# Kernel optimization log

Measured on AMD Instinct MI355X. Metric: run time of the kernel, lower is better.

## Reference

```python
import jax, jax.numpy as jnp
import numpy as np

W_LEN = 10

def _mlp3(x, W1, b1, W2, b2, W3, b3):
    x = jax.nn.relu(x @ W1 + b1)
    x = jax.nn.relu(x @ W2 + b2)
    return x @ W3 + b3

def _make_params(key):
    ks = jax.random.split(key, 16)
    def lin(k, i, o):
        k1, k2 = jax.random.split(k)
        s = 1.0 / np.sqrt(i)
        return (jax.random.uniform(k1, (i, o), jnp.float32, -s, s),
                jax.random.uniform(k2, (o,), jnp.float32, -s, s))
    p = {}
    # encoder: (obs+act)*W = 400 -> 64 -> 64 -> 2
    p['enc_W1'], p['enc_b1'] = lin(ks[0], 400, 64)
    p['enc_W2'], p['enc_b2'] = lin(ks[1], 64, 64)
    p['enc_W3'], p['enc_b3'] = lin(ks[2], 64, 2)
    # GRUCell: input = action+stoch = 10, hidden = det = 2; gates r,z,n
    s = 1.0 / np.sqrt(2)
    p['gru_Wih'] = jax.random.uniform(ks[3], (10, 6), jnp.float32, -s, s)
    p['gru_Whh'] = jax.random.uniform(ks[4], (2, 6), jnp.float32, -s, s)
    p['gru_bih'] = jax.random.uniform(ks[5], (6,), jnp.float32, -s, s)
    p['gru_bhh'] = jax.random.uniform(ks[6], (6,), jnp.float32, -s, s)
    # post_mlp: 2 -> 16 -> 16 -> 2
    p['post_W1'], p['post_b1'] = lin(ks[7], 2, 16)
    p['post_W2'], p['post_b2'] = lin(ks[8], 16, 16)
    p['post_W3'], p['post_b3'] = lin(ks[9], 16, 2)
    # decoder: stoch+action = 10 -> 64 -> 64 -> obs_dim
    p['dec_W1'], p['dec_b1'] = lin(ks[10], 10, 64)
    p['dec_W2'], p['dec_b2'] = lin(ks[11], 64, 64)
    p['dec_W3'], p['dec_b3'] = lin(ks[12], 64, 32)
    return p

def setup_inputs() -> dict:
    key = jax.random.key(0)
    k1, k2, k3, k4, k5 = jax.random.split(key, 5)
    B, T, OD, AD = 512, 512, 32, 8
    N = T - W_LEN + 1
    inp = {
        'obs': jax.random.normal(k1, (B, T, OD), jnp.float32),
        'action': jax.random.normal(k2, (B, T, AD), jnp.float32),
        't_label': jax.random.randint(k3, (B, T), 0, 10, jnp.int32),
        'mask': jax.random.randint(k4, (B, N), 0, 2, jnp.int32),
    }
    inp.update(_make_params(k5))
    return inp

def reference(obs, action, t_label, mask,
              enc_W1, enc_b1, enc_W2, enc_b2, enc_W3, enc_b3,
              gru_Wih, gru_Whh, gru_bih, gru_bhh,
              post_W1, post_b1, post_W2, post_b2, post_W3, post_b3,
              dec_W1, dec_b1, dec_W2, dec_b2, dec_W3, dec_b3):
    B, T, OD = obs.shape
    AD = action.shape[-1]
    N = T - W_LEN + 1
    DET = gru_Whh.shape[0]

    oa = jnp.concatenate([obs, action], axis=-1)            # [B,T,C]
    target_obs_traj = obs[:, W_LEN - 1:, :]                  # [B,N,OD]
    action_traj = action[:, W_LEN - 1:, :]                   # [B,N,AD]
    labels = t_label[:, W_LEN - 1:]

    # torch unfold(1, W, 1): [B,N,C,W] with window along last axis, flatten c-major
    idx = jnp.arange(N)[:, None] + jnp.arange(W_LEN)[None, :]  # [N,W]
    win = oa[:, idx, :]                                      # [B,N,W,C]
    win = jnp.swapaxes(win, 2, 3).reshape(B, N, -1)          # [B,N,C*W]
    priors = _mlp3(win, enc_W1, enc_b1, enc_W2, enc_b2, enc_W3, enc_b3)  # [B,N,S]

    x0 = jnp.zeros((B, DET), obs.dtype)
    s0 = priors[:, 0, :]

    def step(carry, xs):
        x_prev, s_prev = carry
        prior_t, a_t, m_t = xs
        m = m_t[:, None].astype(x_prev.dtype)
        st = m * prior_t + (1.0 - m) * s_prev
        gin = jnp.concatenate([a_t, st], axis=-1)
        gi = gin @ gru_Wih + gru_bih
        gh = x_prev @ gru_Whh + gru_bhh
        ir, iz, inn = jnp.split(gi, 3, axis=-1)
        hr, hz, hn = jnp.split(gh, 3, axis=-1)
        r = jax.nn.sigmoid(ir + hr)
        z = jax.nn.sigmoid(iz + hz)
        n = jnp.tanh(inn + r * hn)
        x_new = (1.0 - z) * n + z * x_prev
        s_new = _mlp3(x_new, post_W1, post_b1, post_W2, post_b2, post_W3, post_b3)
        return (x_new, s_new), (x_new, s_new)

    xs = (jnp.swapaxes(priors[:, :N - 1, :], 0, 1),
          jnp.swapaxes(action_traj[:, :N - 1, :], 0, 1),
          jnp.swapaxes(mask[:, :N - 1], 0, 1))
    _, (x_seq, s_seq) = jax.lax.scan(step, (x0, s0), xs)
    x_traj = jnp.concatenate([x0[:, None, :], jnp.swapaxes(x_seq, 0, 1)], axis=1)  # [B,N,DET]
    posts = jnp.concatenate([s0[:, None, :], jnp.swapaxes(s_seq, 0, 1)], axis=1)   # [B,N,S]

    post_obs_pred = _mlp3(jnp.concatenate([posts, action_traj], axis=-1),
                          dec_W1, dec_b1, dec_W2, dec_b2, dec_W3, dec_b3)          # [B,N,OD]
    return (post_obs_pred, priors, posts, x_traj, target_obs_traj, labels)
```

## Files before the change

kernel.cpp:

```cpp
#include <hip/hip_runtime.h>
#include <hip/hip_bf16.h>

namespace {

constexpr int Bb = 512;
constexpr int Tt = 512;
constexpr int OD = 32;
constexpr int AD = 8;
constexpr int WL = 10;
constexpr int Nn = Tt - WL + 1;
constexpr int CH = OD + AD;
constexpr int REC_T = 512;

constexpr float LOG2E = 1.4426950408889634f;

constexpr long SZ_PO = (long)Bb * Nn * 32;
constexpr long SZ_PR = (long)Bb * Nn * 2;
constexpr long OFF_POST   = 0;
constexpr long OFF_PRIORS = SZ_PO;
constexpr long OFF_POSTS  = OFF_PRIORS + SZ_PR;
constexpr long OFF_XTRAJ  = OFF_POSTS + SZ_PR;
constexpr long OFF_TGT    = OFF_XTRAJ + SZ_PR;
constexpr long OFF_LAB    = OFF_TGT + SZ_PO;

constexpr int PK_W1  = 0;
constexpr int PK_W2  = 26624;
constexpr int PK_W3  = 30720;
constexpr int PK_DW1 = 31744;
constexpr int PK_DW2 = 33792;
constexpr int PK_DW3 = 37888;
constexpr int PK_TOTAL = 39936;

typedef __attribute__((ext_vector_type(8))) short bf16x8;
typedef __attribute__((ext_vector_type(4))) float f32x4;

__device__ __align__(16) short g_pack[PK_TOTAL];

__device__ __forceinline__ f32x4 mfma16(bf16x8 a, bf16x8 b, f32x4 c) {
  return __builtin_amdgcn_mfma_f32_16x16x32_bf16(a, b, c, 0, 0, 0);
}

__device__ __forceinline__ unsigned short f2bf(float x) {
  unsigned int u = __float_as_uint(x);
  unsigned int r = u + 0x7fffu + ((u >> 16) & 1u);
  return (unsigned short)(r >> 16);
}

__device__ __forceinline__ float sigmoidf_(float x) {
  return 1.0f / (1.0f + __expf(-x));
}
__device__ __forceinline__ float tanh_(float x) {
  return 1.0f - 2.0f / (__expf(2.0f * x) + 1.0f);
}

template <int CTRL>
__device__ __forceinline__ float dpp_add(float x) {
  int y = __builtin_amdgcn_update_dpp(0, __float_as_int(x), CTRL, 0xf, 0xf, false);
  return x + __int_as_float(y);
}
template <int CTRL>
__device__ __forceinline__ float dpp_mov(float x) {
  return __int_as_float(
      __builtin_amdgcn_update_dpp(0, __float_as_int(x), CTRL, 0xf, 0xf, false));
}
__device__ __forceinline__ float row16_allsum(float x) {
  x = dpp_add<0xB1>(x);
  x = dpp_add<0x4E>(x);
  x = dpp_add<0x141>(x);
  x = dpp_add<0x140>(x);
  return x;
}

__global__ __launch_bounds__(256) void pack_kernel(
    const float* __restrict__ W1, const float* __restrict__ W2,
    const float* __restrict__ W3, const float* __restrict__ dW1,
    const float* __restrict__ dW2, const float* __restrict__ dW3) {
  const int idx = blockIdx.x * 256 + threadIdx.x;
  if (idx >= PK_TOTAL) return;
  float v = 0.0f;
  int base, r;
  if (idx < PK_W2) {
    base = PK_W1; r = idx - base;
    const int frag = r >> 9, inner = r & 511;
    const int lane = inner >> 3, j = inner & 7;
    const int kb = frag >> 2, jb = frag & 3;
    const int col = lane & 15;
    const int kp = kb * 32 + ((lane >> 4) << 3) + j;
    if (kp < 400) {
      const int w = kp / 40, c = kp - w * 40;
      v = W1[(c * 10 + w) * 64 + jb * 16 + col];
    }
  } else if (idx < PK_W3) {
    base = PK_W2; r = idx - base;
    const int frag = r >> 9, inner = r & 511;
    const int lane = inner >> 3, j = inner & 7;
    const int kb = frag >> 2, jb = frag & 3;
    const int col = lane & 15;
    const int k = kb * 32 + ((lane >> 4) << 3) + j;
    v = W2[k * 64 + jb * 16 + col];
  } else if (idx < PK_DW1) {
    base = PK_W3; r = idx - base;
    const int frag = r >> 9, inner = r & 511;
    const int lane = inner >> 3, j = inner & 7;
    const int kb = frag;
    const int col = lane & 15;
    const int k = kb * 32 + ((lane >> 4) << 3) + j;
    v = (col < 2) ? W3[k * 2 + col] : 0.0f;
  } else if (idx < PK_DW2) {
    base = PK_DW1; r = idx - base;
    const int frag = r >> 9, inner = r & 511;
    const int lane = inner >> 3, j = inner & 7;
    const int jb = frag;
    const int col = lane & 15;
    const int k = ((lane >> 4) << 3) + j;
    v = (k < 10) ? dW1[k * 64 + jb * 16 + col] : 0.0f;
  } else if (idx < PK_DW3) {
    base = PK_DW2; r = idx - base;
    const int frag = r >> 9, inner = r & 511;
    const int lane = inner >> 3, j = inner & 7;
    const int kb = frag >> 2, jb = frag & 3;
    const int col = lane & 15;
    const int k = kb * 32 + ((lane >> 4) << 3) + j;
    v = dW2[k * 64 + jb * 16 + col];
  } else {
    base = PK_DW3; r = idx - base;
    const int frag = r >> 9, inner = r & 511;
    const int lane = inner >> 3, j = inner & 7;
    const int kb = frag >> 1, jb = frag & 1;
    const int col = lane & 15;
    const int k = kb * 32 + ((lane >> 4) << 3) + j;
    v = dW3[k * 32 + jb * 16 + col];
  }
  g_pack[idx] = (short)f2bf(v);
}

__global__ void copy_kernel(const float* __restrict__ obs,
                            const int* __restrict__ tlab,
                            float* __restrict__ out) {
  const int total4 = (int)(SZ_PO / 4);
  const int totalL = Bb * Nn;
  const int stride = gridDim.x * blockDim.x;
  float4* out4 = reinterpret_cast<float4*>(out + OFF_TGT);
  const float4* obs4 = reinterpret_cast<const float4*>(obs);
  for (int idx = blockIdx.x * blockDim.x + threadIdx.x;
       idx < total4 + totalL; idx += stride) {
    if (idx < total4) {
      const int b = idx / (Nn * 8);
      const int r = idx - b * (Nn * 8);
      const int n = r >> 3;
      const int c4 = r & 7;
      out4[idx] = obs4[((long)b * Tt + n + WL - 1) * 8 + c4];
    } else {
      const int j = idx - total4;
      const int b = j / Nn;
      const int n = j - b * Nn;
      out[OFF_LAB + j] = (float)tlab[(long)b * Tt + n + WL - 1];
    }
  }
}

__global__ __launch_bounds__(256) void enc_mfma(
    const float* __restrict__ obs, const float* __restrict__ act,
    const float* __restrict__ b1, const float* __restrict__ b2,
    const float* __restrict__ b3, float* __restrict__ out) {
  __shared__ __align__(16) unsigned short sA[74 * 40];
  __shared__ __align__(16) unsigned short sH1[64 * 64];
  __shared__ __align__(16) unsigned short sH2[64 * 64];
  const int b = blockIdx.x >> 3;
  const int n0 = (blockIdx.x & 7) << 6;
  const int tid = threadIdx.x;
  const int lane = tid & 63, wv = tid >> 6;
  const int q = lane >> 4, lr = lane & 15;
  const int nl = wv * 16 + lr;

  for (int e = tid; e < 74 * 40; e += 256) {
    const int row = e / 40, c = e - row * 40;
    int t = n0 + row; t = t < Tt ? t : Tt - 1;
    const float v = (c < OD) ? obs[((long)b * Tt + t) * OD + c]
                             : act[((long)b * Tt + t) * AD + c - OD];
    sA[e] = f2bf(v);
  }
  __syncthreads();

  const char* sAb = (const char*)sA;
  f32x4 acc[4] = {{0,0,0,0},{0,0,0,0},{0,0,0,0},{0,0,0,0}};
  {
    int c0 = q * 8, w = 0;
#pragma unroll
    for (int kb = 0; kb < 13; ++kb) {
      const bf16x8 a = *(const bf16x8*)(sAb + (nl + w) * 80 + c0 * 2);
#pragma unroll
      for (int jb = 0; jb < 4; ++jb) {
        const bf16x8 bw =
            *(const bf16x8*)&g_pack[PK_W1 + ((kb * 4 + jb) * 64 + lane) * 8];
        acc[jb] = mfma16(a, bw, acc[jb]);
      }
      c0 += 32;
      if (c0 >= 40) { c0 -= 40; ++w; }
    }
  }
  {
#pragma unroll
    for (int jb = 0; jb < 4; ++jb) {
      const float bb = b1[jb * 16 + lr];
#pragma unroll
      for (int r = 0; r < 4; ++r) {
        const int grow = wv * 16 + q * 4 + r;
        const int col = jb * 16 + lr;
        const float v = fmaxf(acc[jb][r] + bb, 0.0f);
        const int byte = (grow * 128 + col * 2) ^ ((grow & 7) << 4);
        *(unsigned short*)((char*)sH1 + byte) = f2bf(v);
      }
    }
  }
  __syncthreads();

  f32x4 ac2[4] = {{0,0,0,0},{0,0,0,0},{0,0,0,0},{0,0,0,0}};
#pragma unroll
  for (int kb = 0; kb < 2; ++kb) {
    const int byte = (nl * 128 + kb * 64 + q * 16) ^ ((lr & 7) << 4);
    const bf16x8 a = *(const bf16x8*)((const char*)sH1 + byte);
#pragma unroll
    for (int jb = 0; jb < 4; ++jb) {
      const bf16x8 bw =
          *(const bf16x8*)&g_pack[PK_W2 + ((kb * 4 + jb) * 64 + lane) * 8];
      ac2[jb] = mfma16(a, bw, ac2[jb]);
    }
  }
  {
#pragma unroll
    for (int jb = 0; jb < 4; ++jb) {
      const float bb = b2[jb * 16 + lr];
#pragma unroll
      for (int r = 0; r < 4; ++r) {
        const int grow = wv * 16 + q * 4 + r;
        const int col = jb * 16 + lr;
        const float v = fmaxf(ac2[jb][r] + bb, 0.0f);
        const int byte = (grow * 128 + col * 2) ^ ((grow & 7) << 4);
        *(unsigned short*)((char*)sH2 + byte) = f2bf(v);
      }
    }
  }
  __syncthreads();

  f32x4 ac3 = {0, 0, 0, 0};
#pragma unroll
  for (int kb = 0; kb < 2; ++kb) {
    const int byte = (nl * 128 + kb * 64 + q * 16) ^ ((lr & 7) << 4);
    const bf16x8 a = *(const bf16x8*)((const char*)sH2 + byte);
    const bf16x8 bw = *(const bf16x8*)&g_pack[PK_W3 + (kb * 64 + lane) * 8];
    ac3 = mfma16(a, bw, ac3);
  }
  if (lr < 2) {
    const float bb = b3[lr];
#pragma unroll
    for (int r = 0; r < 4; ++r) {
      const int grow = wv * 16 + q * 4 + r;
      const int n = n0 + grow;
      if (n < Nn) out[OFF_PRIORS + ((long)b * Nn + n) * 2 + lr] = ac3[r] + bb;
    }
  }
}

__global__ __launch_bounds__(256) void dec_mfma(
    const float* __restrict__ act, const float* __restrict__ b1,
    const float* __restrict__ b2, const float* __restrict__ b3,
    float* __restrict__ out) {
  __shared__ __align__(16) unsigned short sD[64 * 32];
  __shared__ __align__(16) unsigned short sH1[64 * 64];
  __shared__ __align__(16) unsigned short sH2[64 * 64];
  const int b = blockIdx.x >> 3;
  const int n0 = (blockIdx.x & 7) << 6;
  const int tid = threadIdx.x;
  const int lane = tid & 63, wv = tid >> 6;
  const int q = lane >> 4, lr = lane & 15;
  const int nl = wv * 16 + lr;
  const float* posts = out + OFF_POSTS;

  for (int e = tid; e < 64 * 32; e += 256) {
    const int row = e >> 5, c = e & 31;
    int n = n0 + row; n = n < Nn ? n : Nn - 1;
    float v = 0.0f;
    if (c < 2) v = posts[((long)b * Nn + n) * 2 + c];
    else if (c < 10) v = act[((long)b * Tt + n + WL - 1) * AD + c - 2];
    const int byte = (row * 64 + c * 2) ^ ((row & 3) << 4);
    *(unsigned short*)((char*)sD + byte) = f2bf(v);
  }
  __syncthreads();

  f32x4 acc[4] = {{0,0,0,0},{0,0,0,0},{0,0,0,0},{0,0,0,0}};
  {
    const int byte = (nl * 64 + q * 16) ^ ((nl & 3) << 4);
    const bf16x8 a = *(const bf16x8*)((const char*)sD + byte);
#pragma unroll
    for (int jb = 0; jb < 4; ++jb) {
      const bf16x8 bw = *(const bf16x8*)&g_pack[PK_DW1 + (jb * 64 + lane) * 8];
      acc[jb] = mfma16(a, bw, acc[jb]);
    }
  }
  {
#pragma unroll
    for (int jb = 0; jb < 4; ++jb) {
      const float bb = b1[jb * 16 + lr];
#pragma unroll
      for (int r = 0; r < 4; ++r) {
        const int grow = wv * 16 + q * 4 + r;
        const int col = jb * 16 + lr;
        const float v = fmaxf(acc[jb][r] + bb, 0.0f);
        const int byte = (grow * 128 + col * 2) ^ ((grow & 7) << 4);
        *(unsigned short*)((char*)sH1 + byte) = f2bf(v);
      }
    }
  }
  __syncthreads();

  f32x4 ac2[4] = {{0,0,0,0},{0,0,0,0},{0,0,0,0},{0,0,0,0}};
#pragma unroll
  for (int kb = 0; kb < 2; ++kb) {
    const int byte = (nl * 128 + kb * 64 + q * 16) ^ ((lr & 7) << 4);
    const bf16x8 a = *(const bf16x8*)((const char*)sH1 + byte);
#pragma unroll
    for (int jb = 0; jb < 4; ++jb) {
      const bf16x8 bw =
          *(const bf16x8*)&g_pack[PK_DW2 + ((kb * 4 + jb) * 64 + lane) * 8];
      ac2[jb] = mfma16(a, bw, ac2[jb]);
    }
  }
  {
#pragma unroll
    for (int jb = 0; jb < 4; ++jb) {
      const float bb = b2[jb * 16 + lr];
#pragma unroll
      for (int r = 0; r < 4; ++r) {
        const int grow = wv * 16 + q * 4 + r;
        const int col = jb * 16 + lr;
        const float v = fmaxf(ac2[jb][r] + bb, 0.0f);
        const int byte = (grow * 128 + col * 2) ^ ((grow & 7) << 4);
        *(unsigned short*)((char*)sH2 + byte) = f2bf(v);
      }
    }
  }
  __syncthreads();

  f32x4 ac3[2] = {{0,0,0,0},{0,0,0,0}};
#pragma unroll
  for (int kb = 0; kb < 2; ++kb) {
    const int byte = (nl * 128 + kb * 64 + q * 16) ^ ((lr & 7) << 4);
    const bf16x8 a = *(const bf16x8*)((const char*)sH2 + byte);
#pragma unroll
    for (int jb = 0; jb < 2; ++jb) {
      const bf16x8 bw =
          *(const bf16x8*)&g_pack[PK_DW3 + ((kb * 2 + jb) * 64 + lane) * 8];
      ac3[jb] = mfma16(a, bw, ac3[jb]);
    }
  }
#pragma unroll
  for (int jb = 0; jb < 2; ++jb) {
    const int o = jb * 16 + lr;
    const float bb = b3[o];
#pragma unroll
    for (int r = 0; r < 4; ++r) {
      const int grow = wv * 16 + q * 4 + r;
      const int n = n0 + grow;
      if (n < Nn) out[OFF_POST + ((long)b * Nn + n) * 32 + o] = ac3[jb][r] + bb;
    }
  }
}

__global__ __launch_bounds__(256) void gprep_kernel(
    const float* __restrict__ act, const int* __restrict__ mask,
    const float* __restrict__ Wih, const float* __restrict__ bih,
    const float* __restrict__ out, float* __restrict__ rec) {
  const int idx = blockIdx.x * 256 + threadIdx.x;
  const int total = Bb * REC_T;
  if (idx >= total) return;
  const int sub = idx & 3;
  const int t = (idx >> 2) & (REC_T - 1);
  const int blk = idx >> 11;
  const int g = (blk << 2) + sub;
  const float sc[6] = {-LOG2E, -LOG2E, -LOG2E, -LOG2E, 2.f * LOG2E, 2.f * LOG2E};
  float r[12];
#pragma unroll
  for (int i = 0; i < 12; ++i) r[i] = 0.0f;
  if (t < Nn - 1) {
    const float* a = act + ((long)g * Tt + WL - 1 + t) * AD;
    const float4 a0 = *reinterpret_cast<const float4*>(a);
    const float4 a1 = *reinterpret_cast<const float4*>(a + 4);
#pragma unroll
    for (int q = 0; q < 6; ++q) {
      float acc = bih[q];
      acc = fmaf(a0.x, Wih[0 * 6 + q], acc);
      acc = fmaf(a0.y, Wih[1 * 6 + q], acc);
      acc = fmaf(a0.z, Wih[2 * 6 + q], acc);
      acc = fmaf(a0.w, Wih[3 * 6 + q], acc);
      acc = fmaf(a1.x, Wih[4 * 6 + q], acc);
      acc = fmaf(a1.y, Wih[5 * 6 + q], acc);
      acc = fmaf(a1.z, Wih[6 * 6 + q], acc);
      acc = fmaf(a1.w, Wih[7 * 6 + q], acc);
      r[q] = acc * sc[q];
    }
    const float2 pr =
        *reinterpret_cast<const float2*>(out + OFF_PRIORS + ((long)g * Nn + t) * 2);
    r[6] = pr.x;
    r[7] = pr.y;
    r[8] = (float)mask[(long)g * Nn + t];
  }
  float4* o = reinterpret_cast<float4*>(rec + (long)idx * 12);
  o[0] = make_float4(r[0], r[1], r[2], r[3]);
  o[1] = make_float4(r[4], r[5], r[6], r[7]);
  o[2] = make_float4(r[8], r[9], r[10], r[11]);
}

#define SCAN_STEP(GA, GB, MF, TG)                                           \
  do {                                                                      \
    const bool mm = ((MF) != 0.0f);                                         \
    const float st0 = mm ? (GB).z : s0p;                                    \
    const float st1 = mm ? (GB).w : s1p;                                    \
    float giq[6], ghq[6];                                                   \
    _Pragma("unroll") for (int q_ = 0; q_ < 6; ++q_) ghq[q_] =              \
        fmaf(x1p, whh1[q_], fmaf(x0p, whh0[q_], bhhv[q_]));                 \
    giq[0] = fmaf(st1, wih9[0], fmaf(st0, wih8[0], (GA).x));                \
    giq[1] = fmaf(st1, wih9[1], fmaf(st0, wih8[1], (GA).y));                \
    giq[2] = fmaf(st1, wih9[2], fmaf(st0, wih8[2], (GA).z));                \
    giq[3] = fmaf(st1, wih9[3], fmaf(st0, wih8[3], (GA).w));                \
    giq[4] = fmaf(st1, wih9[4], fmaf(st0, wih8[4], (GB).x));                \
    giq[5] = fmaf(st1, wih9[5], fmaf(st0, wih8[5], (GB).y));                \
    const float e0 = __builtin_amdgcn_exp2f(giq[0] + ghq[0]);               \
    const float e1 = __builtin_amdgcn_exp2f(giq[1] + ghq[1]);               \
    const float e2 = __builtin_amdgcn_exp2f(giq[2] + ghq[2]);               \
    const float e3 = __builtin_amdgcn_exp2f(giq[3] + ghq[3]);               \
    const float r0 = __builtin_amdgcn_rcpf(1.0f + e0);                      \
    const float r1 = __builtin_amdgcn_rcpf(1.0f + e1);                      \
    const float z0 = __builtin_amdgcn_rcpf(1.0f + e2);                      \
    const float z1 = __builtin_amdgcn_rcpf(1.0f + e3);                      \
    const float en0 = __builtin_amdgcn_exp2f(fmaf(r0, ghq[4], giq[4]));     \
    const float en1 = __builtin_amdgcn_exp2f(fmaf(r1, ghq[5], giq[5]));     \
    const float nn0 = fmaf(-2.0f, __builtin_amdgcn_rcpf(1.0f + en0), 1.0f); \
    const float nn1 = fmaf(-2.0f, __builtin_amdgcn_rcpf(1.0f + en1), 1.0f); \
    const float xn0 = fmaf(z0, x0p - nn0, nn0);                             \
    const float xn1 = fmaf(z1, x1p - nn1, nn1);                             \
    const float h1 = fmaxf(fmaf(xn1, w1c1, fmaf(xn0, w1c0, b1v)), 0.0f);    \
    const float t0 = h1;                                                    \
    const float t1 = dpp_mov<0xB1>(t0);                                     \
    const float t2 = dpp_mov<0x4E>(t0);                                     \
    const float t3 = dpp_mov<0x4E>(t1);                                     \
    const float t4 = dpp_mov<0x141>(t0);                                    \
    const float t5 = dpp_mov<0x141>(t1);                                    \
    const float t6 = dpp_mov<0x141>(t2);                                    \
    const float t7 = dpp_mov<0x141>(t3);                                    \
    const float t8 = dpp_mov<0x128>(t0);                                    \
    const float t9 = dpp_mov<0x128>(t1);                                    \
    const float t10 = dpp_mov<0x128>(t2);                                   \
    const float t11 = dpp_mov<0x128>(t3);                                   \
    const float t12 = dpp_mov<0x128>(t4);                                   \
    const float t13 = dpp_mov<0x128>(t5);                                   \
    const float t14 = dpp_mov<0x128>(t6);                                   \
    const float t15 = dpp_mov<0x128>(t7);                                   \
    float q0 = fmaf(t0, wg[0], b2v);                                        \
    q0 = fmaf(t1, wg[1], q0);                                               \
    q0 = fmaf(t2, wg[2], q0);                                               \
    q0 = fmaf(t3, wg[3], q0);                                               \
    float q1 = t4 * wg[4];                                                  \
    q1 = fmaf(t5, wg[5], q1);                                               \
    q1 = fmaf(t6, wg[6], q1);                                               \
    q1 = fmaf(t7, wg[7], q1);                                               \
    float q2 = t8 * wg[8];                                                  \
    q2 = fmaf(t9, wg[9], q2);                                               \
    q2 = fmaf(t10, wg[10], q2);                                             \
    q2 = fmaf(t11, wg[11], q2);                                             \
    float q3 = t12 * wg[12];                                                \
    q3 = fmaf(t13, wg[13], q3);                                             \
    q3 = fmaf(t14, wg[14], q3);                                             \
    q3 = fmaf(t15, wg[15], q3);                                             \
    const float h2 = fmaxf((q0 + q1) + (q2 + q3), 0.0f);                    \
    float p0 = row16_allsum(h2 * w3a);                                      \
    float p1 = row16_allsum(h2 * w3b);                                      \
    const float sn0 = p0 + b3a;                                             \
    const float sn1 = p1 + b3b;                                             \
    if (lane == 0 && (TG) < Nn - 1)                                         \
      *reinterpret_cast<float2*>(xw) = make_float2(xn0, xn1);               \
    if (lane == 1 && (TG) < Nn - 1)                                         \
      *reinterpret_cast<float2*>(sw) = make_float2(sn0, sn1);               \
    xw += 2;                                                                \
    sw += 2;                                                                \
    x0p = xn0;                                                              \
    x1p = xn1;                                                              \
    s0p = sn0;                                                              \
    s1p = sn1;                                                              \
  } while (0)

#define LOADCH(C)                                                     \
  do {                                                                \
    const float* p_ = gsrc + (C) * 768 + tid * 12;                    \
    st0 = *reinterpret_cast<const float4*>(p_);                       \
    st1 = *reinterpret_cast<const float4*>(p_ + 4);                   \
    st2 = *reinterpret_cast<const float4*>(p_ + 8);                   \
  } while (0)
#define WRITECH(BUF)                                                  \
  do {                                                                \
    float* q_ = &slds[BUF][tid * 12];                                 \
    *reinterpret_cast<float4*>(q_) = st0;                             \
    *reinterpret_cast<float4*>(q_ + 4) = st1;                         \
    *reinterpret_cast<float4*>(q_ + 8) = st2;                         \
  } while (0)

__global__ __launch_bounds__(64, 1) void scan4_kernel(
    const float* __restrict__ rec, const float* __restrict__ pW2,
    const float* __restrict__ pW1, const float* __restrict__ pb1,
    const float* __restrict__ pb2, const float* __restrict__ pW3,
    const float* __restrict__ pb3, const float* __restrict__ Wih,
    const float* __restrict__ Whh, const float* __restrict__ bhh,
    float* __restrict__ out) {
  __shared__ __align__(16) float slds[2][768];
  const int tid = threadIdx.x;
  const int lane = tid & 15;
  const int sub = tid >> 4;
  const int blk = blockIdx.x;
  const int g = (blk << 2) + sub;

  const float sc[6] = {-LOG2E, -LOG2E, -LOG2E, -LOG2E, 2.f * LOG2E, 2.f * LOG2E};
  float wih8[6], wih9[6], whh0[6], whh1[6], bhhv[6];
#pragma unroll
  for (int q = 0; q < 6; ++q) {
    wih8[q] = Wih[8 * 6 + q] * sc[q];
    wih9[q] = Wih[9 * 6 + q] * sc[q];
    whh0[q] = Whh[q] * sc[q];
    whh1[q] = Whh[6 + q] * sc[q];
    bhhv[q] = bhh[q] * sc[q];
  }
  const float w1c0 = pW1[lane], w1c1 = pW1[16 + lane], b1v = pb1[lane];
  constexpr int otab[16] = {0, 1, 2, 3, 7, 6, 5, 4, 8, 9, 10, 11, 15, 14, 13, 12};
  float wg[16];
#pragma unroll
  for (int i = 0; i < 16; ++i) wg[i] = pW2[(lane ^ otab[i]) * 16 + lane];
  const float b2v = pb2[lane];
  const float w3a = pW3[lane * 2], w3b = pW3[lane * 2 + 1];
  const float b3a = pb3[0], b3b = pb3[1];

  const float* priors = out + OFF_PRIORS;
  const long pbase = (long)g * Nn;
  const float* gsrc = rec + (long)blk * (REC_T * 48);
  float* xw = out + OFF_XTRAJ + pbase * 2 + 2;
  float* sw = out + OFF_POSTS + pbase * 2 + 2;

  const float2 s0v = *reinterpret_cast<const float2*>(priors + pbase * 2);
  float x0p = 0.f, x1p = 0.f;
  float s0p = s0v.x, s1p = s0v.y;
  if (lane == 0)
    *reinterpret_cast<float2*>(out + OFF_XTRAJ + pbase * 2) =
        make_float2(0.f, 0.f);
  if (lane == 1)
    *reinterpret_cast<float2*>(out + OFF_POSTS + pbase * 2) =
        make_float2(s0p, s1p);

  float4 st0, st1, st2;
  LOADCH(0);
  WRITECH(0);
  LOADCH(1);

  float4 cGA, cGB;
  float cMF;
  {
    const float* rp = &slds[0][(sub)*12];
    cGA = *reinterpret_cast<const float4*>(rp);
    cGB = *reinterpret_cast<const float4*>(rp + 4);
    cMF = rp[8];
  }

  int tg = 0;
  for (int c = 0; c < 32; ++c) {
    const int buf = c & 1;
    if (c + 1 < 32) WRITECH((c + 1) & 1);
    if (c + 2 < 32) LOADCH(c + 2);
#pragma unroll
    for (int tl = 0; tl < 16; ++tl) {
      const float4 GA = cGA;
      const float4 GB = cGB;
      const float MF = cMF;
      const int ntl = (tl + 1) & 15;
      const int nbuf = (tl == 15) ? (buf ^ 1) : buf;
      const float* rp = &slds[nbuf][(ntl * 4 + sub) * 12];
      cGA = *reinterpret_cast<const float4*>(rp);
      cGB = *reinterpret_cast<const float4*>(rp + 4);
      cMF = rp[8];
      SCAN_STEP(GA, GB, MF, tg);
      ++tg;
    }
  }
}

__global__ __launch_bounds__(64) void scan_fb_kernel(
    const float* __restrict__ act, const int* __restrict__ mask,
    const float* __restrict__ Wih, const float* __restrict__ Whh,
    const float* __restrict__ bih, const float* __restrict__ bhh,
    const float* __restrict__ pW1, const float* __restrict__ pb1,
    const float* __restrict__ pW2, const float* __restrict__ pb2,
    const float* __restrict__ pW3, const float* __restrict__ pb3,
    float* __restrict__ out) {
  const int tid = threadIdx.x;
  const int lane = tid & 15;
  const int g = (blockIdx.x * 64 + tid) >> 4;

  float wih8[6], wih9[6], whh0[6], whh1[6], bhhv[6], bihv[6];
  float wihA[8][6];
#pragma unroll
  for (int q = 0; q < 6; ++q) {
    wih8[q] = Wih[8 * 6 + q];
    wih9[q] = Wih[9 * 6 + q];
    whh0[q] = Whh[q];
    whh1[q] = Whh[6 + q];
    bhhv[q] = bhh[q];
    bihv[q] = bih[q];
  }
#pragma unroll
  for (int i = 0; i < 8; ++i)
#pragma unroll
    for (int q = 0; q < 6; ++q) wihA[i][q] = Wih[i * 6 + q];

  const float w1c0 = pW1[lane], w1c1 = pW1[16 + lane], b1v = pb1[lane];
  float w2c[16];
#pragma unroll
  for (int k = 0; k < 16; ++k) w2c[k] = pW2[k * 16 + lane];
  const float b2v = pb2[lane];
  const float w3a = pW3[lane * 2], w3b = pW3[lane * 2 + 1];
  const float b3a = pb3[0], b3b = pb3[1];

  const float* priors = out + OFF_PRIORS;
  float* posts = out + OFF_POSTS;
  float* xtraj = out + OFF_XTRAJ;
  const long pbase = (long)g * Nn;
  const float* aptr = act + ((long)g * Tt + WL - 1) * 8;

  const float2 s0v = *reinterpret_cast<const float2*>(priors + pbase * 2);
  float x0p = 0.f, x1p = 0.f;
  float s0p = s0v.x, s1p = s0v.y;
  if (lane == 0)
    *reinterpret_cast<float2*>(xtraj + pbase * 2) = make_float2(0.f, 0.f);
  if (lane == 1)
    *reinterpret_cast<float2*>(posts + pbase * 2) = make_float2(s0p, s1p);

  float4 an0 = *reinterpret_cast<const float4*>(aptr);
  float4 an1 = *reinterpret_cast<const float4*>(aptr + 4);
  float2 prn = s0v;
  int mn = mask[pbase];

  for (int t = 0; t < Nn - 1; ++t) {
    const float4 a0 = an0, a1 = an1;
    const float2 pr = prn;
    const int m = mn;
    const int tn1 = (t + 1 < Nn - 1) ? t + 1 : Nn - 2;
    an0 = *reinterpret_cast<const float4*>(aptr + (long)tn1 * 8);
    an1 = *reinterpret_cast<const float4*>(aptr + (long)tn1 * 8 + 4);
    prn = *reinterpret_cast<const float2*>(priors + (pbase + t + 1) * 2);
    mn = mask[pbase + t + 1];

    const float st0 = m ? pr.x : s0p;
    const float st1 = m ? pr.y : s1p;

    float giq[6], ghq[6];
#pragma unroll
    for (int q = 0; q < 6; ++q) {
      float acc = bihv[q];
      acc = fmaf(a0.x, wihA[0][q], acc);
      acc = fmaf(a0.y, wihA[1][q], acc);
      acc = fmaf(a0.z, wihA[2][q], acc);
      acc = fmaf(a0.w, wihA[3][q], acc);
      acc = fmaf(a1.x, wihA[4][q], acc);
      acc = fmaf(a1.y, wihA[5][q], acc);
      acc = fmaf(a1.z, wihA[6][q], acc);
      acc = fmaf(a1.w, wihA[7][q], acc);
      giq[q] = fmaf(st1, wih9[q], fmaf(st0, wih8[q], acc));
      ghq[q] = fmaf(x1p, whh1[q], fmaf(x0p, whh0[q], bhhv[q]));
    }
    const float r0 = sigmoidf_(giq[0] + ghq[0]);
    const float r1 = sigmoidf_(giq[1] + ghq[1]);
    const float z0 = sigmoidf_(giq[2] + ghq[2]);
    const float z1 = sigmoidf_(giq[3] + ghq[3]);
    const float nn0 = tanh_(fmaf(r0, ghq[4], giq[4]));
    const float nn1 = tanh_(fmaf(r1, ghq[5], giq[5]));
    const float xn0 = fmaf(z0, x0p - nn0, nn0);
    const float xn1 = fmaf(z1, x1p - nn1, nn1);

    const float h1 = fmaxf(fmaf(xn1, w1c1, fmaf(xn0, w1c0, b1v)), 0.0f);
    float ha[16];
#pragma unroll
    for (int k = 0; k < 16; ++k) ha[k] = __shfl(h1, k, 16);
    float q0 = fmaf(ha[0], w2c[0], b2v);
    q0 = fmaf(ha[1], w2c[1], q0);
    q0 = fmaf(ha[2], w2c[2], q0);
    q0 = fmaf(ha[3], w2c[3], q0);
    float q1 = ha[4] * w2c[4];
    q1 = fmaf(ha[5], w2c[5], q1);
    q1 = fmaf(ha[6], w2c[6], q1);
    q1 = fmaf(ha[7], w2c[7], q1);
    float q2 = ha[8] * w2c[8];
    q2 = fmaf(ha[9], w2c[9], q2);
    q2 = fmaf(ha[10], w2c[10], q2);
    q2 = fmaf(ha[11], w2c[11], q2);
    float q3 = ha[12] * w2c[12];
    q3 = fmaf(ha[13], w2c[13], q3);
    q3 = fmaf(ha[14], w2c[14], q3);
    q3 = fmaf(ha[15], w2c[15], q3);
    const float h2 = fmaxf((q0 + q1) + (q2 + q3), 0.0f);

    float p0 = row16_allsum(h2 * w3a);
    float p1 = row16_allsum(h2 * w3b);
    const float sn0 = p0 + b3a;
    const float sn1 = p1 + b3b;

    if (lane == 0)
      *reinterpret_cast<float2*>(xtraj + (pbase + t + 1) * 2) =
          make_float2(xn0, xn1);
    if (lane == 1)
      *reinterpret_cast<float2*>(posts + (pbase + t + 1) * 2) =
          make_float2(sn0, sn1);
    x0p = xn0; x1p = xn1; s0p = sn0; s1p = sn1;
  }
}

}

extern "C" void kernel_launch(void* const* d_in, const int* in_sizes, int n_in,
                              void* d_out, int out_size, void* d_ws, size_t ws_size,
                              hipStream_t stream) {
  const float* obs    = (const float*)d_in[0];
  const float* action = (const float*)d_in[1];
  const int* t_label  = (const int*)d_in[2];
  const int* mask     = (const int*)d_in[3];
  const float* enc_W1 = (const float*)d_in[4];
  const float* enc_b1 = (const float*)d_in[5];
  const float* enc_W2 = (const float*)d_in[6];
  const float* enc_b2 = (const float*)d_in[7];
  const float* enc_W3 = (const float*)d_in[8];
  const float* enc_b3 = (const float*)d_in[9];
  const float* gru_Wih = (const float*)d_in[10];
  const float* gru_Whh = (const float*)d_in[11];
  const float* gru_bih = (const float*)d_in[12];
  const float* gru_bhh = (const float*)d_in[13];
  const float* post_W1 = (const float*)d_in[14];
  const float* post_b1 = (const float*)d_in[15];
  const float* post_W2 = (const float*)d_in[16];
  const float* post_b2 = (const float*)d_in[17];
  const float* post_W3 = (const float*)d_in[18];
  const float* post_b3 = (const float*)d_in[19];
  const float* dec_W1 = (const float*)d_in[20];
  const float* dec_b1 = (const float*)d_in[21];
  const float* dec_W2 = (const float*)d_in[22];
  const float* dec_b2 = (const float*)d_in[23];
  const float* dec_W3 = (const float*)d_in[24];
  const float* dec_b3 = (const float*)d_in[25];
  float* out = (float*)d_out;

  pack_kernel<<<(PK_TOTAL + 255) / 256, 256, 0, stream>>>(
      enc_W1, enc_W2, enc_W3, dec_W1, dec_W2, dec_W3);

  enc_mfma<<<Bb * 8, 256, 0, stream>>>(obs, action, enc_b1, enc_b2, enc_b3,
                                       out);

  const size_t rec_bytes = (size_t)Bb * REC_T * 12 * sizeof(float);
  if (ws_size >= rec_bytes) {
    float* rec = (float*)d_ws;
    const int total = Bb * REC_T;
    gprep_kernel<<<(total + 255) / 256, 256, 0, stream>>>(
        action, mask, gru_Wih, gru_bih, out, rec);
    scan4_kernel<<<128, 64, 0, stream>>>(rec, post_W2, post_W1, post_b1,
                                         post_b2, post_W3, post_b3, gru_Wih,
                                         gru_Whh, gru_bhh, out);
  } else {
    scan_fb_kernel<<<128, 64, 0, stream>>>(
        action, mask, gru_Wih, gru_Whh, gru_bih, gru_bhh, post_W1, post_b1,
        post_W2, post_b2, post_W3, post_b3, out);
  }

  dec_mfma<<<Bb * 8, 256, 0, stream>>>(action, dec_b1, dec_b2, dec_b3, out);
  copy_kernel<<<2048, 256, 0, stream>>>(obs, t_label, out);
}
```

Baseline: 249.4 us.

## Interleave four independent GRU sequences per lane group in the scan kernel

The recurrent scan kernel now advances four independent batch sequences per 16-lane group, so each wave handles 16 sequences instead of 4. The grid drops from 128 to 32 blocks. The gprep record layout is re-indexed to match, and the per-step LDS prefetch is replicated for the four chains. The aim is to hide the long serial exp/rcp/DPP dependency chain of each step with instruction-level parallelism across independent sequences. The cost is that each wave issues four times the work per step, on a quarter as many waves, with higher register pressure.

Result: slower. 697.2 us (+179.6%).

```diff
diff --git a/kernel.cpp b/kernel.cpp
--- a/kernel.cpp
+++ b/kernel.cpp
@@ -374,10 +374,10 @@
   const int idx = blockIdx.x * 256 + threadIdx.x;
   const int total = Bb * REC_T;
   if (idx >= total) return;
-  const int sub = idx & 3;
-  const int t = (idx >> 2) & (REC_T - 1);
-  const int blk = idx >> 11;
-  const int g = (blk << 2) + sub;
+  const int c16 = idx & 15;
+  const int t = (idx >> 4) & (REC_T - 1);
+  const int blk = idx >> 13;
+  const int g = (blk << 4) + c16;
   const float sc[6] = {-LOG2E, -LOG2E, -LOG2E, -LOG2E, 2.f * LOG2E, 2.f * LOG2E};
   float r[12];
 #pragma unroll
@@ -411,14 +411,14 @@
   o[2] = make_float4(r[8], r[9], r[10], r[11]);
 }
 
-#define SCAN_STEP(GA, GB, MF, TG)                                           \
+#define SCAN_STEP(GA, GB, MF, TG, X0, X1, S0, S1, XW, SW, LX, LS)           \
   do {                                                                      \
     const bool mm = ((MF) != 0.0f);                                         \
-    const float st0 = mm ? (GB).z : s0p;                                    \
-    const float st1 = mm ? (GB).w : s1p;                                    \
+    const float st0 = mm ? (GB).z : S0;                                     \
+    const float st1 = mm ? (GB).w : S1;                                     \
     float giq[6], ghq[6];                                                   \
     _Pragma("unroll") for (int q_ = 0; q_ < 6; ++q_) ghq[q_] =              \
-        fmaf(x1p, whh1[q_], fmaf(x0p, whh0[q_], bhhv[q_]));                 \
+        fmaf(X1, whh1[q_], fmaf(X0, whh0[q_], bhhv[q_]));                   \
     giq[0] = fmaf(st1, wih9[0], fmaf(st0, wih8[0], (GA).x));                \
     giq[1] = fmaf(st1, wih9[1], fmaf(st0, wih8[1], (GA).y));                \
     giq[2] = fmaf(st1, wih9[2], fmaf(st0, wih8[2], (GA).z));                \
@@ -437,8 +437,8 @@
     const float en1 = __builtin_amdgcn_exp2f(fmaf(r1, ghq[5], giq[5]));     \
     const float nn0 = fmaf(-2.0f, __builtin_amdgcn_rcpf(1.0f + en0), 1.0f); \
     const float nn1 = fmaf(-2.0f, __builtin_amdgcn_rcpf(1.0f + en1), 1.0f); \
-    const float xn0 = fmaf(z0, x0p - nn0, nn0);                             \
-    const float xn1 = fmaf(z1, x1p - nn1, nn1);                             \
+    const float xn0 = fmaf(z0, X0 - nn0, nn0);                              \
+    const float xn1 = fmaf(z1, X1 - nn1, nn1);                              \
     const float h1 = fmaxf(fmaf(xn1, w1c1, fmaf(xn0, w1c0, b1v)), 0.0f);    \
     const float t0 = h1;                                                    \
     const float t1 = dpp_mov<0xB1>(t0);                                     \
@@ -477,16 +477,16 @@
     float p1 = row16_allsum(h2 * w3b);                                      \
     const float sn0 = p0 + b3a;                                             \
     const float sn1 = p1 + b3b;                                             \
-    if (lane == 0 && (TG) < Nn - 1)                                         \
-      *reinterpret_cast<float2*>(xw) = make_float2(xn0, xn1);               \
-    if (lane == 1 && (TG) < Nn - 1)                                         \
-      *reinterpret_cast<float2*>(sw) = make_float2(sn0, sn1);               \
-    xw += 2;                                                                \
-    sw += 2;                                                                \
-    x0p = xn0;                                                              \
-    x1p = xn1;                                                              \
-    s0p = sn0;                                                              \
-    s1p = sn1;                                                              \
+    if (lane == (LX) && (TG) < Nn - 1)                                      \
+      *reinterpret_cast<float2*>(XW) = make_float2(xn0, xn1);               \
+    if (lane == (LS) && (TG) < Nn - 1)                                      \
+      *reinterpret_cast<float2*>(SW) = make_float2(sn0, sn1);               \
+    XW += 2;                                                                \
+    SW += 2;                                                                \
+    X0 = xn0;                                                               \
+    X1 = xn1;                                                               \
+    S0 = sn0;                                                               \
+    S1 = sn1;                                                               \
   } while (0)
 
 #define LOADCH(C)                                                     \
@@ -503,8 +503,15 @@
     *reinterpret_cast<float4*>(q_ + 4) = st1;                         \
     *reinterpret_cast<float4*>(q_ + 8) = st2;                         \
   } while (0)
-
-__global__ __launch_bounds__(64, 1) void scan4_kernel(
+#define PFSTEP(CGA, CGB, CMF, NB, NT, C16)                            \
+  do {                                                                \
+    const float* rp_ = &slds[NB][(((NT)*16) + (C16)) * 12];           \
+    CGA = *reinterpret_cast<const float4*>(rp_);                      \
+    CGB = *reinterpret_cast<const float4*>(rp_ + 4);                  \
+    CMF = rp_[8];                                                     \
+  } while (0)
+
+__global__ __launch_bounds__(64, 1) void scan5_kernel(
     const float* __restrict__ rec, const float* __restrict__ pW2,
     const float* __restrict__ pW1, const float* __restrict__ pb1,
     const float* __restrict__ pb2, const float* __restrict__ pW3,
@@ -516,7 +523,10 @@
   const int lane = tid & 15;
   const int sub = tid >> 4;
   const int blk = blockIdx.x;
-  const int g = (blk << 2) + sub;
+  const int gA = (blk << 4) + sub;
+  const int gB = gA + 4;
+  const int gC = gA + 8;
+  const int gD = gA + 12;
 
   const float sc[6] = {-LOG2E, -LOG2E, -LOG2E, -LOG2E, 2.f * LOG2E, 2.f * LOG2E};
   float wih8[6], wih9[6], whh0[6], whh1[6], bhhv[6];
@@ -538,52 +548,80 @@
   const float b3a = pb3[0], b3b = pb3[1];
 
   const float* priors = out + OFF_PRIORS;
-  const long pbase = (long)g * Nn;
-  const float* gsrc = rec + (long)blk * (REC_T * 48);
-  float* xw = out + OFF_XTRAJ + pbase * 2 + 2;
-  float* sw = out + OFF_POSTS + pbase * 2 + 2;
-
-  const float2 s0v = *reinterpret_cast<const float2*>(priors + pbase * 2);
-  float x0p = 0.f, x1p = 0.f;
-  float s0p = s0v.x, s1p = s0v.y;
-  if (lane == 0)
-    *reinterpret_cast<float2*>(out + OFF_XTRAJ + pbase * 2) =
-        make_float2(0.f, 0.f);
-  if (lane == 1)
-    *reinterpret_cast<float2*>(out + OFF_POSTS + pbase * 2) =
-        make_float2(s0p, s1p);
+  const float* gsrc = rec + (long)blk * (REC_T * 192);
+
+  float* xwA = out + OFF_XTRAJ + (long)gA * Nn * 2 + 2;
+  float* swA = out + OFF_POSTS + (long)gA * Nn * 2 + 2;
+  float* xwB = out + OFF_XTRAJ + (long)gB * Nn * 2 + 2;
+  float* swB = out + OFF_POSTS + (long)gB * Nn * 2 + 2;
+  float* xwC = out + OFF_XTRAJ + (long)gC * Nn * 2 + 2;
+  float* swC = out + OFF_POSTS + (long)gC * Nn * 2 + 2;
+  float* xwD = out + OFF_XTRAJ + (long)gD * Nn * 2 + 2;
+  float* swD = out + OFF_POSTS + (long)gD * Nn * 2 + 2;
+
+  float x0A = 0.f, x1A = 0.f, s0A, s1A;
+  float x0B = 0.f, x1B = 0.f, s0B, s1B;
+  float x0C = 0.f, x1C = 0.f, s0C, s1C;
+  float x0D = 0.f, x1D = 0.f, s0D, s1D;
+  {
+    const float2 a = *reinterpret_cast<const float2*>(priors + (long)gA * Nn * 2);
+    const float2 b = *reinterpret_cast<const float2*>(priors + (long)gB * Nn * 2);
+    const float2 c = *reinterpret_cast<const float2*>(priors + (long)gC * Nn * 2);
+    const float2 d = *reinterpret_cast<const float2*>(priors + (long)gD * Nn * 2);
+    s0A = a.x; s1A = a.y; s0B = b.x; s1B = b.y;
+    s0C = c.x; s1C = c.y; s0D = d.x; s1D = d.y;
+    if (lane == 0) {
+      *reinterpret_cast<float2*>(out + OFF_XTRAJ + (long)gA * Nn * 2) = make_float2(0.f, 0.f);
+      *reinterpret_cast<float2*>(out + OFF_POSTS + (long)gA * Nn * 2) = a;
+    }
+    if (lane == 1) {
+      *reinterpret_cast<float2*>(out + OFF_XTRAJ + (long)gB * Nn * 2) = make_float2(0.f, 0.f);
+      *reinterpret_cast<float2*>(out + OFF_POSTS + (long)gB * Nn * 2) = b;
+    }
+    if (lane == 2) {
+      *reinterpret_cast<float2*>(out + OFF_XTRAJ + (long)gC * Nn * 2) = make_float2(0.f, 0.f);
+      *reinterpret_cast<float2*>(out + OFF_POSTS + (long)gC * Nn * 2) = c;
+    }
+    if (lane == 3) {
+      *reinterpret_cast<float2*>(out + OFF_XTRAJ + (long)gD * Nn * 2) = make_float2(0.f, 0.f);
+      *reinterpret_cast<float2*>(out + OFF_POSTS + (long)gD * Nn * 2) = d;
+    }
+  }
 
   float4 st0, st1, st2;
   LOADCH(0);
   WRITECH(0);
   LOADCH(1);
 
-  float4 cGA, cGB;
-  float cMF;
-  {
-    const float* rp = &slds[0][(sub)*12];
-    cGA = *reinterpret_cast<const float4*>(rp);
-    cGB = *reinterpret_cast<const float4*>(rp + 4);
-    cMF = rp[8];
-  }
+  float4 cGAa, cGBa, cGAb, cGBb, cGAc, cGBc, cGAd, cGBd;
+  float cMFa, cMFb, cMFc, cMFd;
+  PFSTEP(cGAa, cGBa, cMFa, 0, 0, sub);
+  PFSTEP(cGAb, cGBb, cMFb, 0, 0, sub + 4);
+  PFSTEP(cGAc, cGBc, cMFc, 0, 0, sub + 8);
+  PFSTEP(cGAd, cGBd, cMFd, 0, 0, sub + 12);
 
   int tg = 0;
-  for (int c = 0; c < 32; ++c) {
+  for (int c = 0; c < 128; ++c) {
     const int buf = c & 1;
-    if (c + 1 < 32) WRITECH((c + 1) & 1);
-    if (c + 2 < 32) LOADCH(c + 2);
-#pragma unroll
-    for (int tl = 0; tl < 16; ++tl) {
-      const float4 GA = cGA;
-      const float4 GB = cGB;
-      const float MF = cMF;
-      const int ntl = (tl + 1) & 15;
-      const int nbuf = (tl == 15) ? (buf ^ 1) : buf;
-      const float* rp = &slds[nbuf][(ntl * 4 + sub) * 12];
-      cGA = *reinterpret_cast<const float4*>(rp);
-      cGB = *reinterpret_cast<const float4*>(rp + 4);
-      cMF = rp[8];
-      SCAN_STEP(GA, GB, MF, tg);
+    if (c + 1 < 128) WRITECH((c + 1) & 1);
+    if (c + 2 < 128) LOADCH(c + 2);
+#pragma unroll
+    for (int tl = 0; tl < 4; ++tl) {
+      const float4 GAa = cGAa, GBa = cGBa;
+      const float4 GAb = cGAb, GBb = cGBb;
+      const float4 GAc = cGAc, GBc = cGBc;
+      const float4 GAd = cGAd, GBd = cGBd;
+      const float MFa = cMFa, MFb = cMFb, MFc = cMFc, MFd = cMFd;
+      const int ntl = (tl + 1) & 3;
+      const int nbuf = (tl == 3) ? (buf ^ 1) : buf;
+      PFSTEP(cGAa, cGBa, cMFa, nbuf, ntl, sub);
+      PFSTEP(cGAb, cGBb, cMFb, nbuf, ntl, sub + 4);
+      PFSTEP(cGAc, cGBc, cMFc, nbuf, ntl, sub + 8);
+      PFSTEP(cGAd, cGBd, cMFd, nbuf, ntl, sub + 12);
+      SCAN_STEP(GAa, GBa, MFa, tg, x0A, x1A, s0A, s1A, xwA, swA, 0, 1);
+      SCAN_STEP(GAb, GBb, MFb, tg, x0B, x1B, s0B, s1B, xwB, swB, 2, 3);
+      SCAN_STEP(GAc, GBc, MFc, tg, x0C, x1C, s0C, s1C, xwC, swC, 4, 5);
+      SCAN_STEP(GAd, GBd, MFd, tg, x0D, x1D, s0D, s1D, xwD, swD, 6, 7);
       ++tg;
     }
   }
@@ -763,9 +801,9 @@
     const int total = Bb * REC_T;
     gprep_kernel<<<(total + 255) / 256, 256, 0, stream>>>(
         action, mask, gru_Wih, gru_bih, out, rec);
-    scan4_kernel<<<128, 64, 0, stream>>>(rec, post_W2, post_W1, post_b1,
-                                         post_b2, post_W3, post_b3, gru_Wih,
-                                         gru_Whh, gru_bhh, out);
+    scan5_kernel<<<32, 64, 0, stream>>>(rec, post_W2, post_W1, post_b1,
+                                        post_b2, post_W3, post_b3, gru_Wih,
+                                        gru_Whh, gru_bhh, out);
   } else {
     scan_fb_kernel<<<128, 64, 0, stream>>>(
         action, mask, gru_Wih, gru_Whh, gru_bih, gru_bhh, post_W1, post_b1,
```

## Fold target/label copy into scan kernel's idle CUs to overlap with serial scan

Applied to the files above, without the earlier changes.

The serial GRU scan uses only 128 single-wave blocks, which leaves most CUs idle. This change adds 2048 extra blocks to the scan launch that perform the target-obs and label copy, removing the separate copy kernel launch and hiding its memory traffic behind the latency-bound scan. The risk is that the copy blocks compete for memory bandwidth or scheduling with the scan blocks, which are on the critical path. The copy now uses 64-thread blocks instead of 256-thread ones.

New measurement: 240.6 us. 3.5% less time.

```diff
diff --git a/kernel.cpp b/kernel.cpp
--- a/kernel.cpp
+++ b/kernel.cpp
@@ -510,9 +510,35 @@
     const float* __restrict__ pb2, const float* __restrict__ pW3,
     const float* __restrict__ pb3, const float* __restrict__ Wih,
     const float* __restrict__ Whh, const float* __restrict__ bhh,
+    const float* __restrict__ obs, const int* __restrict__ tlab,
     float* __restrict__ out) {
   __shared__ __align__(16) float slds[2][768];
   const int tid = threadIdx.x;
+
+  if (blockIdx.x >= 128) {
+    const int total4 = (int)(SZ_PO / 4);
+    const int totalL = Bb * Nn;
+    const int stride = (gridDim.x - 128) * 64;
+    float4* out4 = reinterpret_cast<float4*>(out + OFF_TGT);
+    const float4* obs4 = reinterpret_cast<const float4*>(obs);
+    for (int idx = (blockIdx.x - 128) * 64 + tid; idx < total4 + totalL;
+         idx += stride) {
+      if (idx < total4) {
+        const int b = idx / (Nn * 8);
+        const int r = idx - b * (Nn * 8);
+        const int n = r >> 3;
+        const int c4 = r & 7;
+        out4[idx] = obs4[((long)b * Tt + n + WL - 1) * 8 + c4];
+      } else {
+        const int j = idx - total4;
+        const int b = j / Nn;
+        const int n = j - b * Nn;
+        out[OFF_LAB + j] = (float)tlab[(long)b * Tt + n + WL - 1];
+      }
+    }
+    return;
+  }
+
   const int lane = tid & 15;
   const int sub = tid >> 4;
   const int blk = blockIdx.x;
@@ -763,15 +789,15 @@
     const int total = Bb * REC_T;
     gprep_kernel<<<(total + 255) / 256, 256, 0, stream>>>(
         action, mask, gru_Wih, gru_bih, out, rec);
-    scan4_kernel<<<128, 64, 0, stream>>>(rec, post_W2, post_W1, post_b1,
-                                         post_b2, post_W3, post_b3, gru_Wih,
-                                         gru_Whh, gru_bhh, out);
+    scan4_kernel<<<128 + 2048, 64, 0, stream>>>(
+        rec, post_W2, post_W1, post_b1, post_b2, post_W3, post_b3, gru_Wih,
+        gru_Whh, gru_bhh, obs, t_label, out);
   } else {
     scan_fb_kernel<<<128, 64, 0, stream>>>(
         action, mask, gru_Wih, gru_Whh, gru_bih, gru_bhh, post_W1, post_b1,
         post_W2, post_b2, post_W3, post_b3, out);
+    copy_kernel<<<2048, 256, 0, stream>>>(obs, t_label, out);
   }
 
   dec_mfma<<<Bb * 8, 256, 0, stream>>>(action, dec_b1, dec_b2, dec_b3, out);
-  copy_kernel<<<2048, 256, 0, stream>>>(obs, t_label, out);
-}
+}
```
